# Kernel tuning notes

Hardware: AMD Instinct MI355X
Metric: run time of the kernel (lower is better)

## Reference

```python
import jax, jax.numpy as jnp
import numpy as np

B, S, H = 4, 1024, 1024
NH, HD = 16, 64  # num heads, head dim


def setup_inputs() -> dict:
    key = jax.random.key(0)
    ks = jax.random.split(key, 7)
    scale = 1.0 / np.sqrt(H)
    return {
        "hidden_states": jax.random.normal(ks[0], (B, S, H), jnp.float32),
        "attention_mask": jnp.zeros((B, 1, 1, S), jnp.float32),
        "Wq": jax.random.normal(ks[1], (H, H), jnp.float32) * scale,
        "bq": jnp.zeros((H,), jnp.float32),
        "Wk": jax.random.normal(ks[2], (H, H), jnp.float32) * scale,
        "bk": jnp.zeros((H,), jnp.float32),
        "Wv": jax.random.normal(ks[3], (H, H), jnp.float32) * scale,
        "bv": jnp.zeros((H,), jnp.float32),
    }


def _heads(x):
    # [B,S,H] -> [B,NH,S,HD]
    return x.reshape(x.shape[0], x.shape[1], NH, HD).transpose(0, 2, 1, 3)


def reference(hidden_states, attention_mask, Wq, bq, Wk, bk, Wv, bv):
    q = _heads(hidden_states @ Wq + bq)  # [B,NH,S,HD]
    k = _heads(hidden_states @ Wk + bk)
    v = _heads(hidden_states @ Wv + bv)
    scores = jnp.einsum("bhqd,bhkd->bhqk", q, k) / np.sqrt(HD)
    scores = scores + attention_mask  # broadcast additive mask
    probs = jax.nn.softmax(scores, axis=-1)  # dropout p=0 (eval)
    ctx = jnp.einsum("bhqk,bhkd->bhqd", probs, v)
    # [B,NH,S,HD] -> [B,S,H]
    return ctx.transpose(0, 2, 1, 3).reshape(hidden_states.shape[0], hidden_states.shape[1], NH * HD)
```

## Files before the change

kernel.cpp:

```cpp
#include <hip/hip_runtime.h>
#include <hip/hip_bf16.h>

typedef __bf16 bf16_t;
typedef __bf16 bf16x8 __attribute__((ext_vector_type(8)));
typedef float f32x4 __attribute__((ext_vector_type(4)));
typedef float f32x8 __attribute__((ext_vector_type(8)));
typedef float f32x16 __attribute__((ext_vector_type(16)));
typedef unsigned uint2v __attribute__((ext_vector_type(2)));

#define MFMA16(a, b, c) __builtin_amdgcn_mfma_f32_16x16x32_bf16((a), (b), (c), 0, 0, 0)
#define MFMA32(a, b, c) __builtin_amdgcn_mfma_f32_32x32x16_bf16((a), (b), (c), 0, 0, 0)

static constexpr int BB = 4, SS = 1024, HH = 1024, NHEAD = 16, HDIM = 64;
static constexpr int MM = BB * SS;

__device__ __forceinline__ void gload_lds16(const void* g, void* l) {
  __builtin_amdgcn_global_load_lds((const __attribute__((address_space(1))) void*)g,
                                   (__attribute__((address_space(3))) void*)l, 16, 0, 0);
}

#if __has_builtin(__builtin_amdgcn_permlane32_swap)
#define PSWAP(a, b)                                                    \
  {                                                                    \
    uint2v _r = __builtin_amdgcn_permlane32_swap((a), (b), false, false); \
    (a) = _r.x;                                                        \
    (b) = _r.y;                                                        \
  }
#else
#define PSWAP(a, b) asm("v_permlane32_swap_b32 %0, %1" : "+v"(a), "+v"(b))
#endif

__device__ __forceinline__ float EXP2(float x) {
  float r;
  asm("v_exp_f32 %0, %1" : "=v"(r) : "v"(x));
  return r;
}

__global__ __launch_bounds__(256) void prep_kernel(const float* __restrict__ hs,
                                                   const float* __restrict__ Wq,
                                                   const float* __restrict__ Wk,
                                                   const float* __restrict__ Wv,
                                                   bf16_t* __restrict__ hiddenB,
                                                   bf16_t* __restrict__ WT) {
  const int t = threadIdx.x;
  if (blockIdx.x < 2048) {
    int i = (blockIdx.x * 256 + t) * 8;
    float4 a = *(const float4*)(hs + i);
    float4 b = *(const float4*)(hs + i + 4);
    union { int4 i4; bf16_t h[8]; } u;
    u.h[0] = (bf16_t)a.x; u.h[1] = (bf16_t)a.y; u.h[2] = (bf16_t)a.z; u.h[3] = (bf16_t)a.w;
    u.h[4] = (bf16_t)b.x; u.h[5] = (bf16_t)b.y; u.h[6] = (bf16_t)b.z; u.h[7] = (bf16_t)b.w;
    *(int4*)(hiddenB + i) = u.i4;
  } else {
    __shared__ float tile[32][33];
    int id = blockIdx.x - 2048;
    int z = id >> 10;
    int rem = id & 1023;
    int bx = rem & 31, by = rem >> 5;
    const float* W = (z == 0) ? Wq : (z == 1) ? Wk : Wv;
    bf16_t* Out = WT + (size_t)z * HH * HH;
    int tx = t & 31, ty = t >> 5;
    int x0 = bx * 32;
    int y0 = by * 32;
    for (int j = ty; j < 32; j += 8)
      tile[j][tx] = W[(size_t)(y0 + j) * HH + x0 + tx];
    __syncthreads();
    for (int j = ty; j < 32; j += 8)
      Out[(size_t)(x0 + j) * HH + y0 + tx] = (bf16_t)tile[tx][j];
  }
}

#define BMT 128
#define BNT 384
#define BKT 64
#define NTL 16
#define BUFBYTES 65536

__global__ __launch_bounds__(512, 2) void qkv_gemm5(const bf16_t* __restrict__ hiddenB,
                                                    const bf16_t* __restrict__ WT,
                                                    const float* __restrict__ bq,
                                                    const float* __restrict__ bk,
                                                    const float* __restrict__ bv,
                                                    bf16_t* __restrict__ Qo,
                                                    bf16_t* __restrict__ Ko,
                                                    bf16_t* __restrict__ Vt) {
  __shared__ bf16_t smem[2 * BUFBYTES / 2];

  const int wg = blockIdx.x;
  const int id = (wg & 7) * 32 + (wg >> 3);
  const int nb = id & 7;
  const int mb = id >> 3;

  const int t = threadIdx.x;
  const int lane = t & 63;
  const int w = t >> 6;
  const int wr = w >> 2;
  const int wc = w & 3;
  const int lr = lane & 15;
  const int g4 = lane >> 4;

  const unsigned schunk = (((unsigned)(t & 7)) ^ ((unsigned)((t >> 3) & 7))) << 4;
  const char* Ag = (const char*)hiddenB + (size_t)(mb * BMT) * 2048;
  const char* Bg = (const char*)WT + (size_t)(nb * BNT) * 2048;

  auto stage = [&](const char* gb, int growbase, int kbyte, char* ldsdest) {
    gload_lds16(gb + (size_t)(growbase + (t >> 3)) * 2048 + kbyte + schunk,
                ldsdest + w * 1024);
  };
  const unsigned axor = ((unsigned)(lr & 7)) << 4;

  auto rdA = [&](const char* Ab, int mi, int ks) -> bf16x8 {
    return *(const bf16x8*)(Ab + (size_t)(wr * 64 + mi * 16 + lr) * 128 +
                            (((unsigned)(ks * 64 + g4 * 16)) ^ axor));
  };
  auto rdB = [&](const char* Bb, int p, int ni, int ks) -> bf16x8 {
    return *(const bf16x8*)(Bb + (size_t)(p * 128 + wc * 32 + ni * 16 + lr) * 128 +
                            (((unsigned)(ks * 64 + g4 * 16)) ^ axor));
  };

  f32x4 acc[4][6] = {};

  {
    char* S0 = (char*)smem;
    stage(Ag, 0, 0, S0); stage(Ag, 64, 0, S0 + 8192);
#pragma unroll
    for (int i = 0; i < 6; ++i) stage(Bg, i * 64, 0, S0 + 16384 + i * 8192);
    char* S1 = (char*)smem + BUFBYTES;
    stage(Ag, 0, 128, S1); stage(Ag, 64, 128, S1 + 8192);
#pragma unroll
    for (int i = 0; i < 6; ++i) stage(Bg, i * 64, 128, S1 + 16384 + i * 8192);
  }
  asm volatile("s_waitcnt vmcnt(8)" ::: "memory");
  __builtin_amdgcn_s_barrier();

  for (int j = 0; j < NTL; ++j) {
    const char* Ab = (const char*)smem + (j & 1) * BUFBYTES;
    const char* Bb = Ab + 16384;
    char* Sb = (char*)smem + (j & 1) * BUFBYTES;
    const bool st = (j + 2 < NTL);
    const int kb2 = (j + 2) * 128;

    bf16x8 af[4][2], b0[2][2];
#pragma unroll
    for (int mi = 0; mi < 4; ++mi)
#pragma unroll
      for (int ks = 0; ks < 2; ++ks) af[mi][ks] = rdA(Ab, mi, ks);
#pragma unroll
    for (int ni = 0; ni < 2; ++ni)
#pragma unroll
      for (int ks = 0; ks < 2; ++ks) b0[ni][ks] = rdB(Bb, 0, ni, ks);
    asm volatile("s_waitcnt lgkmcnt(0)" ::: "memory");
    __builtin_amdgcn_s_barrier();
    if (st) {
      stage(Ag, 0, kb2, Sb); stage(Ag, 64, kb2, Sb + 8192);
      stage(Bg, 0, kb2, Sb + 16384); stage(Bg, 64, kb2, Sb + 16384 + 8192);
    }
    __builtin_amdgcn_s_setprio(1);
#pragma unroll
    for (int mi = 0; mi < 4; ++mi)
#pragma unroll
      for (int ni = 0; ni < 2; ++ni)
#pragma unroll
        for (int ks = 0; ks < 2; ++ks)
          acc[mi][ni] = MFMA16(af[mi][ks], b0[ni][ks], acc[mi][ni]);
    __builtin_amdgcn_s_setprio(0);

    bf16x8 b1[2][2];
#pragma unroll
    for (int ni = 0; ni < 2; ++ni)
#pragma unroll
      for (int ks = 0; ks < 2; ++ks) b1[ni][ks] = rdB(Bb, 1, ni, ks);
    asm volatile("s_waitcnt lgkmcnt(0)" ::: "memory");
    __builtin_amdgcn_s_barrier();
    if (st) {
      stage(Bg, 128, kb2, Sb + 16384 + 2 * 8192);
      stage(Bg, 192, kb2, Sb + 16384 + 3 * 8192);
    }
    __builtin_amdgcn_s_setprio(1);
#pragma unroll
    for (int mi = 0; mi < 4; ++mi)
#pragma unroll
      for (int ni = 0; ni < 2; ++ni)
#pragma unroll
        for (int ks = 0; ks < 2; ++ks)
          acc[mi][2 + ni] = MFMA16(af[mi][ks], b1[ni][ks], acc[mi][2 + ni]);
    __builtin_amdgcn_s_setprio(0);

    bf16x8 b2[2][2];
#pragma unroll
    for (int ni = 0; ni < 2; ++ni)
#pragma unroll
      for (int ks = 0; ks < 2; ++ks) b2[ni][ks] = rdB(Bb, 2, ni, ks);
    asm volatile("s_waitcnt lgkmcnt(0)" ::: "memory");
    __builtin_amdgcn_s_barrier();
    if (st) {
      stage(Bg, 256, kb2, Sb + 16384 + 4 * 8192);
      stage(Bg, 320, kb2, Sb + 16384 + 5 * 8192);
    }
    __builtin_amdgcn_s_setprio(1);
#pragma unroll
    for (int mi = 0; mi < 4; ++mi)
#pragma unroll
      for (int ni = 0; ni < 2; ++ni)
#pragma unroll
        for (int ks = 0; ks < 2; ++ks)
          acc[mi][4 + ni] = MFMA16(af[mi][ks], b2[ni][ks], acc[mi][4 + ni]);
    __builtin_amdgcn_s_setprio(0);

    if (j + 1 < NTL) {
      if (st)
        asm volatile("s_waitcnt vmcnt(8)" ::: "memory");
      else
        asm volatile("s_waitcnt vmcnt(0)" ::: "memory");
      __builtin_amdgcn_s_barrier();
    }
  }

#pragma unroll
  for (int ni6 = 0; ni6 < 6; ++ni6) {
    int p = ni6 >> 1, ni = ni6 & 1;
    int col = nb * BNT + p * 128 + wc * 32 + ni * 16 + lr;
    int z = col >> 10;
    int ci = col & 1023;
    const float* bias = (z == 0) ? bq : (z == 1) ? bk : bv;
    float bia = bias[ci];
    int hh = ci >> 6, d = ci & 63;
    if (z < 2) {
      bf16_t* Out = (z == 0) ? Qo : Ko;
#pragma unroll
      for (int mi = 0; mi < 4; ++mi) {
#pragma unroll
        for (int r = 0; r < 4; ++r) {
          int row = mb * BMT + wr * 64 + mi * 16 + g4 * 4 + r;
          int b = row >> 10, s = row & 1023;
          Out[((size_t)(b * NHEAD + hh) * SS + s) * HDIM + d] = (bf16_t)(acc[mi][ni6][r] + bia);
        }
      }
    } else {
#pragma unroll
      for (int mi = 0; mi < 4; ++mi) {
        int row0 = mb * BMT + wr * 64 + mi * 16 + g4 * 4;
        int b = row0 >> 10, s0 = row0 & 1023;
        float v0 = acc[mi][ni6][0] + bia, v1 = acc[mi][ni6][1] + bia;
        float v2 = acc[mi][ni6][2] + bia, v3 = acc[mi][ni6][3] + bia;
        unsigned u0, u1;
        asm("v_cvt_pk_bf16_f32 %0, %1, %2" : "=v"(u0) : "v"(v0), "v"(v1));
        asm("v_cvt_pk_bf16_f32 %0, %1, %2" : "=v"(u1) : "v"(v2), "v"(v3));
        uint2 pv; pv.x = u0; pv.y = u1;
        *(uint2*)&Vt[((size_t)(b * NHEAD + hh) * HDIM + d) * SS + s0] = pv;
      }
    }
  }
}

__global__ __launch_bounds__(512, 4) void attn8_kernel(const bf16_t* __restrict__ Q,
                                                       const bf16_t* __restrict__ K,
                                                       const bf16_t* __restrict__ Vt,
                                                       const float* __restrict__ mask,
                                                       float* __restrict__ out) {
  __shared__ bf16_t KVsm[2][2][2][64 * 64];
  __shared__ float Msm[SS];

  const int wg = blockIdx.x;
  const int id = (wg & 7) * 64 + (wg >> 3);
  const int xblk = id & 7;
  const int bh = id >> 3;

  const int b = bh >> 4;
  const int h = bh & 15;
  const int t = threadIdx.x;
  const int lane = t & 63;
  const int w = t >> 6;
  const int wl = w & 3;
  const int half = w >> 2;
  const int l31 = lane & 31;
  const int hi = lane >> 5;
  const int q0 = xblk * 128 + wl * 32;
  const int kvbase = half * 512;

  const bf16_t* Qh = Q + (size_t)bh * SS * HDIM;
  const bf16_t* Kh = K + (size_t)bh * SS * HDIM;
  const bf16_t* Vh = Vt + (size_t)bh * HDIM * SS;

  const float L2E = 1.4426950408889634f;
  if (t < 256) {
    float4 mv = *(const float4*)&mask[(size_t)b * SS + t * 4];
    mv.x = mv.x * L2E - 16.f; mv.y = mv.y * L2E - 16.f;
    mv.z = mv.z * L2E - 16.f; mv.w = mv.w * L2E - 16.f;
    *(float4*)&Msm[t * 4] = mv;
  }

  bf16x8 qb[4];
#pragma unroll
  for (int c = 0; c < 4; ++c) {
    bf16x8 q = *(const bf16x8*)&Qh[(size_t)(q0 + l31) * HDIM + c * 16 + hi * 8];
#pragma unroll
    for (int e = 0; e < 8; ++e) q[e] = (bf16_t)((float)q[e] * (0.125f * L2E));
    qb[c] = q;
  }

  const int srow = lane >> 3;
  const unsigned gcol = ((lane & 7) * 16) ^ (srow << 4);
  const unsigned swz = (unsigned)((l31 & 7) << 4);

  auto stageKV = [&](int tile, int buf) {
    const int kv0 = kvbase + tile * 64;
#pragma unroll
    for (int i = 0; i < 2; ++i) {
      int rbase = wl * 16 + i * 8;
      gload_lds16((const char*)Kh + (size_t)(kv0 + rbase + srow) * 128 + gcol,
                  (char*)&KVsm[half][buf][0][0] + (size_t)rbase * 128);
      gload_lds16((const char*)Vh + (size_t)(rbase + srow) * 2048 + (size_t)kv0 * 2 + gcol,
                  (char*)&KVsm[half][buf][1][0] + (size_t)rbase * 128);
    }
  };

  f32x16 acc0 = {}, acc1 = {};
  f32x8 la = {}, lb = {};

  stageKV(0, 0);
  asm volatile("s_waitcnt vmcnt(0) lgkmcnt(0)" ::: "memory");
  __builtin_amdgcn_s_barrier();

  for (int tt = 0; tt < 8; ++tt) {
    if (tt + 1 < 8) stageKV(tt + 1, (tt + 1) & 1);
    const char* Kb = (const char*)&KVsm[half][tt & 1][0][0];
    const char* Vb = (const char*)&KVsm[half][tt & 1][1][0];
    const int kv0 = kvbase + tt * 64;

    f32x16 st0 = {}, st1 = {};
    __builtin_amdgcn_s_setprio(1);
#pragma unroll
    for (int c = 0; c < 4; ++c) {
      bf16x8 kf0 = *(const bf16x8*)(Kb + (size_t)l31 * 128 + ((unsigned)(c * 32 + hi * 16) ^ swz));
      st0 = MFMA32(kf0, qb[c], st0);
    }
#pragma unroll
    for (int c = 0; c < 4; ++c) {
      bf16x8 kf1 = *(const bf16x8*)(Kb + (size_t)(32 + l31) * 128 + ((unsigned)(c * 32 + hi * 16) ^ swz));
      st1 = MFMA32(kf1, qb[c], st1);
    }
    __builtin_amdgcn_s_setprio(0);

#pragma unroll
    for (int k2 = 0; k2 < 8; ++k2) {
      int off = 8 * (k2 >> 1) + 4 * hi + 2 * (k2 & 1);
      float2 m0v = *(const float2*)&Msm[kv0 + off];
      float2 m1v = *(const float2*)&Msm[kv0 + 32 + off];
      st0[2 * k2] += m0v.x; st0[2 * k2 + 1] += m0v.y;
      st1[2 * k2] += m1v.x; st1[2 * k2 + 1] += m1v.y;
    }
#pragma unroll
    for (int r = 0; r < 16; ++r) st0[r] = EXP2(st0[r]);
#pragma unroll
    for (int r = 0; r < 16; ++r) st1[r] = EXP2(st1[r]);

#pragma unroll
    for (int r = 0; r < 8; ++r) {
      la[r] += st0[r] + st0[r + 8];
      lb[r] += st1[r] + st1[r + 8];
    }

    unsigned wd0[8], wd1[8];
#pragma unroll
    for (int k2 = 0; k2 < 8; ++k2) {
      unsigned r0, r1;
      float a0f = st0[2 * k2], a1f = st0[2 * k2 + 1];
      float b0f = st1[2 * k2], b1f = st1[2 * k2 + 1];
      asm("v_cvt_pk_bf16_f32 %0, %1, %2" : "=v"(r0) : "v"(a0f), "v"(a1f));
      asm("v_cvt_pk_bf16_f32 %0, %1, %2" : "=v"(r1) : "v"(b0f), "v"(b1f));
      wd0[k2] = r0; wd1[k2] = r1;
    }
    unsigned a0 = wd0[0], b0 = wd0[2]; PSWAP(a0, b0);
    unsigned a1 = wd0[1], b1 = wd0[3]; PSWAP(a1, b1);
    unsigned a2 = wd0[4], b2 = wd0[6]; PSWAP(a2, b2);
    unsigned a3 = wd0[5], b3 = wd0[7]; PSWAP(a3, b3);
    unsigned c0 = wd1[0], d0 = wd1[2]; PSWAP(c0, d0);
    unsigned c1 = wd1[1], d1 = wd1[3]; PSWAP(c1, d1);
    unsigned c2 = wd1[4], d2 = wd1[6]; PSWAP(c2, d2);
    unsigned c3 = wd1[5], d3 = wd1[7]; PSWAP(c3, d3);
    union { unsigned u[4]; bf16x8 v; } pf0, pf1, pf2, pf3;
    pf0.u[0] = a0; pf0.u[1] = a1; pf0.u[2] = b0; pf0.u[3] = b1;
    pf1.u[0] = a2; pf1.u[1] = a3; pf1.u[2] = b2; pf1.u[3] = b3;
    pf2.u[0] = c0; pf2.u[1] = c1; pf2.u[2] = d0; pf2.u[3] = d1;
    pf3.u[0] = c2; pf3.u[1] = c3; pf3.u[2] = d2; pf3.u[3] = d3;

    __builtin_amdgcn_s_setprio(1);
    {
      bf16x8 vf;
      vf = *(const bf16x8*)(Vb + (size_t)(l31) * 128 + ((unsigned)(0 * 32 + hi * 16) ^ swz));
      acc0 = MFMA32(vf, pf0.v, acc0);
      vf = *(const bf16x8*)(Vb + (size_t)(32 + l31) * 128 + ((unsigned)(0 * 32 + hi * 16) ^ swz));
      acc1 = MFMA32(vf, pf0.v, acc1);
      vf = *(const bf16x8*)(Vb + (size_t)(l31) * 128 + ((unsigned)(1 * 32 + hi * 16) ^ swz));
      acc0 = MFMA32(vf, pf1.v, acc0);
      vf = *(const bf16x8*)(Vb + (size_t)(32 + l31) * 128 + ((unsigned)(1 * 32 + hi * 16) ^ swz));
      acc1 = MFMA32(vf, pf1.v, acc1);
      vf = *(const bf16x8*)(Vb + (size_t)(l31) * 128 + ((unsigned)(2 * 32 + hi * 16) ^ swz));
      acc0 = MFMA32(vf, pf2.v, acc0);
      vf = *(const bf16x8*)(Vb + (size_t)(32 + l31) * 128 + ((unsigned)(2 * 32 + hi * 16) ^ swz));
      acc1 = MFMA32(vf, pf2.v, acc1);
      vf = *(const bf16x8*)(Vb + (size_t)(l31) * 128 + ((unsigned)(3 * 32 + hi * 16) ^ swz));
      acc0 = MFMA32(vf, pf3.v, acc0);
      vf = *(const bf16x8*)(Vb + (size_t)(32 + l31) * 128 + ((unsigned)(3 * 32 + hi * 16) ^ swz));
      acc1 = MFMA32(vf, pf3.v, acc1);
    }
    __builtin_amdgcn_s_setprio(0);

    asm volatile("s_waitcnt vmcnt(0)" ::: "memory");
    __builtin_amdgcn_s_barrier();
  }

  float l_run;
  {
    float s0 = (la[0] + lb[0]) + (la[1] + lb[1]);
    float s1 = (la[2] + lb[2]) + (la[3] + lb[3]);
    float s2 = (la[4] + lb[4]) + (la[5] + lb[5]);
    float s3 = (la[6] + lb[6]) + (la[7] + lb[7]);
    l_run = (s0 + s1) + (s2 + s3);
    l_run += __shfl_xor(l_run, 32);
  }

  __syncthreads();
  float* mb = (float*)&KVsm[0][0][0][0];
  if (half == 1) {
    float* dst = mb + ((size_t)(wl * 64 + lane)) * 36;
#pragma unroll
    for (int g = 0; g < 4; ++g) {
      float4 w0, w1;
      w0.x = acc0[g * 4 + 0]; w0.y = acc0[g * 4 + 1];
      w0.z = acc0[g * 4 + 2]; w0.w = acc0[g * 4 + 3];
      w1.x = acc1[g * 4 + 0]; w1.y = acc1[g * 4 + 1];
      w1.z = acc1[g * 4 + 2]; w1.w = acc1[g * 4 + 3];
      *(float4*)(dst + g * 4) = w0;
      *(float4*)(dst + 16 + g * 4) = w1;
    }
    dst[32] = l_run;
  }
  __syncthreads();
  if (half == 0) {
    const float* src = mb + ((size_t)(wl * 64 + lane)) * 36;
    float rinv = 1.0f / (l_run + src[32]);
    int q = q0 + l31;
    float* ob = out + ((size_t)(b * SS + q)) * HH + h * HDIM;
#pragma unroll
    for (int g = 0; g < 4; ++g) {
      float4 o0, o1;
      o0.x = (acc0[g * 4 + 0] + src[g * 4 + 0]) * rinv;
      o0.y = (acc0[g * 4 + 1] + src[g * 4 + 1]) * rinv;
      o0.z = (acc0[g * 4 + 2] + src[g * 4 + 2]) * rinv;
      o0.w = (acc0[g * 4 + 3] + src[g * 4 + 3]) * rinv;
      o1.x = (acc1[g * 4 + 0] + src[16 + g * 4 + 0]) * rinv;
      o1.y = (acc1[g * 4 + 1] + src[16 + g * 4 + 1]) * rinv;
      o1.z = (acc1[g * 4 + 2] + src[16 + g * 4 + 2]) * rinv;
      o1.w = (acc1[g * 4 + 3] + src[16 + g * 4 + 3]) * rinv;
      *(float4*)&ob[g * 8 + 4 * hi] = o0;
      *(float4*)&ob[32 + g * 8 + 4 * hi] = o1;
    }
  }
}

extern "C" void kernel_launch(void* const* d_in, const int* in_sizes, int n_in,
                              void* d_out, int out_size, void* d_ws, size_t ws_size,
                              hipStream_t stream) {
  const float* hs   = (const float*)d_in[0];
  const float* mask = (const float*)d_in[1];
  const float* Wq   = (const float*)d_in[2];
  const float* bq   = (const float*)d_in[3];
  const float* Wk   = (const float*)d_in[4];
  const float* bk   = (const float*)d_in[5];
  const float* Wv   = (const float*)d_in[6];
  const float* bv   = (const float*)d_in[7];
  float* out = (float*)d_out;

  char* ws = (char*)d_ws;
  bf16_t* hiddenB = (bf16_t*)ws;
  bf16_t* WT      = (bf16_t*)(ws + (size_t)8 * 1024 * 1024);
  bf16_t* Qb      = (bf16_t*)(ws + (size_t)14 * 1024 * 1024);
  bf16_t* Kb      = (bf16_t*)(ws + (size_t)22 * 1024 * 1024);
  bf16_t* Vt      = (bf16_t*)(ws + (size_t)30 * 1024 * 1024);

  prep_kernel<<<2048 + 3072, 256, 0, stream>>>(hs, Wq, Wk, Wv, hiddenB, WT);
  qkv_gemm5<<<256, 512, 0, stream>>>(hiddenB, WT, bq, bk, bv, Qb, Kb, Vt);
  attn8_kernel<<<512, 512, 0, stream>>>(Qb, Kb, Vt, mask, out);
}
```

Measured before the change: 70.79 us.

## Fuse fp32-to-bf16 conversion of hidden states into the QKV GEMM loader

The hidden-state conversion pass is removed from the prep kernel. The QKV GEMM now loads fp32 activations directly into registers, converts them to bf16 with packed cvt instructions, and writes them into swizzled LDS, while B tiles keep using direct global-to-LDS loads. This avoids a separate write and re-read of an 8 MB bf16 intermediate. In exchange the GEMM reads twice as many A bytes, holds extra registers for the in-flight fp32 data, and adjusts its vmcnt wait counts.

```diff
diff --git a/kernel.cpp b/kernel.cpp
--- a/kernel.cpp
+++ b/kernel.cpp
@@ -35,48 +35,40 @@
   asm("v_exp_f32 %0, %1" : "=v"(r) : "v"(x));
   return r;
 }
-
-__global__ __launch_bounds__(256) void prep_kernel(const float* __restrict__ hs,
-                                                   const float* __restrict__ Wq,
-                                                   const float* __restrict__ Wk,
-                                                   const float* __restrict__ Wv,
-                                                   bf16_t* __restrict__ hiddenB,
-                                                   bf16_t* __restrict__ WT) {
+__device__ __forceinline__ unsigned CVTPK(float lo, float hi) {
+  unsigned r;
+  asm("v_cvt_pk_bf16_f32 %0, %1, %2" : "=v"(r) : "v"(lo), "v"(hi));
+  return r;
+}
+
+__global__ __launch_bounds__(256) void prepW_kernel(const float* __restrict__ Wq,
+                                                    const float* __restrict__ Wk,
+                                                    const float* __restrict__ Wv,
+                                                    bf16_t* __restrict__ WT) {
+  __shared__ float tile[32][33];
   const int t = threadIdx.x;
-  if (blockIdx.x < 2048) {
-    int i = (blockIdx.x * 256 + t) * 8;
-    float4 a = *(const float4*)(hs + i);
-    float4 b = *(const float4*)(hs + i + 4);
-    union { int4 i4; bf16_t h[8]; } u;
-    u.h[0] = (bf16_t)a.x; u.h[1] = (bf16_t)a.y; u.h[2] = (bf16_t)a.z; u.h[3] = (bf16_t)a.w;
-    u.h[4] = (bf16_t)b.x; u.h[5] = (bf16_t)b.y; u.h[6] = (bf16_t)b.z; u.h[7] = (bf16_t)b.w;
-    *(int4*)(hiddenB + i) = u.i4;
-  } else {
-    __shared__ float tile[32][33];
-    int id = blockIdx.x - 2048;
-    int z = id >> 10;
-    int rem = id & 1023;
-    int bx = rem & 31, by = rem >> 5;
-    const float* W = (z == 0) ? Wq : (z == 1) ? Wk : Wv;
-    bf16_t* Out = WT + (size_t)z * HH * HH;
-    int tx = t & 31, ty = t >> 5;
-    int x0 = bx * 32;
-    int y0 = by * 32;
-    for (int j = ty; j < 32; j += 8)
-      tile[j][tx] = W[(size_t)(y0 + j) * HH + x0 + tx];
-    __syncthreads();
-    for (int j = ty; j < 32; j += 8)
-      Out[(size_t)(x0 + j) * HH + y0 + tx] = (bf16_t)tile[tx][j];
-  }
+  int id = blockIdx.x;
+  int z = id >> 10;
+  int rem = id & 1023;
+  int bx = rem & 31, by = rem >> 5;
+  const float* W = (z == 0) ? Wq : (z == 1) ? Wk : Wv;
+  bf16_t* Out = WT + (size_t)z * HH * HH;
+  int tx = t & 31, ty = t >> 5;
+  int x0 = bx * 32;
+  int y0 = by * 32;
+  for (int j = ty; j < 32; j += 8)
+    tile[j][tx] = W[(size_t)(y0 + j) * HH + x0 + tx];
+  __syncthreads();
+  for (int j = ty; j < 32; j += 8)
+    Out[(size_t)(x0 + j) * HH + y0 + tx] = (bf16_t)tile[tx][j];
 }
 
 #define BMT 128
 #define BNT 384
-#define BKT 64
 #define NTL 16
 #define BUFBYTES 65536
 
-__global__ __launch_bounds__(512, 2) void qkv_gemm5(const bf16_t* __restrict__ hiddenB,
+__global__ __launch_bounds__(512, 2) void qkv_gemm6(const float* __restrict__ hs,
                                                     const bf16_t* __restrict__ WT,
                                                     const float* __restrict__ bq,
                                                     const float* __restrict__ bk,
@@ -99,16 +91,31 @@
   const int lr = lane & 15;
   const int g4 = lane >> 4;
 
-  const unsigned schunk = (((unsigned)(t & 7)) ^ ((unsigned)((t >> 3) & 7))) << 4;
-  const char* Ag = (const char*)hiddenB + (size_t)(mb * BMT) * 2048;
+  const int srow8 = t >> 3;
+  const int chunk = t & 7;
+  const unsigned schunk = (((unsigned)chunk) ^ ((unsigned)(srow8 & 7))) << 4;
+  const char* Ag32 = (const char*)hs + (size_t)(mb * BMT) * 4096;
   const char* Bg = (const char*)WT + (size_t)(nb * BNT) * 2048;
 
-  auto stage = [&](const char* gb, int growbase, int kbyte, char* ldsdest) {
-    gload_lds16(gb + (size_t)(growbase + (t >> 3)) * 2048 + kbyte + schunk,
+  auto stageB = [&](int growbase, int kbyte, char* ldsdest) {
+    gload_lds16(Bg + (size_t)(growbase + srow8) * 2048 + kbyte + schunk,
                 ldsdest + w * 1024);
   };
+  auto loadA = [&](int u, int kt, float4* dst) {
+    const char* p = Ag32 + (size_t)(u * 64 + srow8) * 4096 + (size_t)kt * 256 + chunk * 32;
+    dst[0] = *(const float4*)p;
+    dst[1] = *(const float4*)(p + 16);
+  };
+  auto writeA = [&](int u, const float4* a, char* SbA) {
+    uint4 wv;
+    wv.x = CVTPK(a[0].x, a[0].y);
+    wv.y = CVTPK(a[0].z, a[0].w);
+    wv.z = CVTPK(a[1].x, a[1].y);
+    wv.w = CVTPK(a[1].z, a[1].w);
+    *(uint4*)(SbA + (size_t)u * 8192 + (size_t)srow8 * 128 + schunk) = wv;
+  };
+
   const unsigned axor = ((unsigned)(lr & 7)) << 4;
-
   auto rdA = [&](const char* Ab, int mi, int ks) -> bf16x8 {
     return *(const bf16x8*)(Ab + (size_t)(wr * 64 + mi * 16 + lr) * 128 +
                             (((unsigned)(ks * 64 + g4 * 16)) ^ axor));
@@ -121,17 +128,21 @@
   f32x4 acc[4][6] = {};
 
   {
+    float4 pa0[2][2], pa1[2][2];
+    loadA(0, 0, pa0[0]); loadA(1, 0, pa0[1]);
+    loadA(0, 1, pa1[0]); loadA(1, 1, pa1[1]);
     char* S0 = (char*)smem;
-    stage(Ag, 0, 0, S0); stage(Ag, 64, 0, S0 + 8192);
-#pragma unroll
-    for (int i = 0; i < 6; ++i) stage(Bg, i * 64, 0, S0 + 16384 + i * 8192);
     char* S1 = (char*)smem + BUFBYTES;
-    stage(Ag, 0, 128, S1); stage(Ag, 64, 128, S1 + 8192);
-#pragma unroll
-    for (int i = 0; i < 6; ++i) stage(Bg, i * 64, 128, S1 + 16384 + i * 8192);
-  }
-  asm volatile("s_waitcnt vmcnt(8)" ::: "memory");
-  __builtin_amdgcn_s_barrier();
+#pragma unroll
+    for (int i = 0; i < 6; ++i) stageB(i * 64, 0, S0 + 16384 + i * 8192);
+#pragma unroll
+    for (int i = 0; i < 6; ++i) stageB(i * 64, 128, S1 + 16384 + i * 8192);
+    writeA(0, pa0[0], S0); writeA(1, pa0[1], S0);
+    writeA(0, pa1[0], S1); writeA(1, pa1[1], S1);
+    asm volatile("s_waitcnt lgkmcnt(0)" ::: "memory");
+    asm volatile("s_waitcnt vmcnt(6)" ::: "memory");
+    __builtin_amdgcn_s_barrier();
+  }
 
   for (int j = 0; j < NTL; ++j) {
     const char* Ab = (const char*)smem + (j & 1) * BUFBYTES;
@@ -140,6 +151,7 @@
     const bool st = (j + 2 < NTL);
     const int kb2 = (j + 2) * 128;
 
+    float4 a32[2][2];
     bf16x8 af[4][2], b0[2][2];
 #pragma unroll
     for (int mi = 0; mi < 4; ++mi)
@@ -152,8 +164,9 @@
     asm volatile("s_waitcnt lgkmcnt(0)" ::: "memory");
     __builtin_amdgcn_s_barrier();
     if (st) {
-      stage(Ag, 0, kb2, Sb); stage(Ag, 64, kb2, Sb + 8192);
-      stage(Bg, 0, kb2, Sb + 16384); stage(Bg, 64, kb2, Sb + 16384 + 8192);
+      loadA(0, j + 2, a32[0]);
+      loadA(1, j + 2, a32[1]);
+      stageB(0, kb2, Sb + 16384); stageB(64, kb2, Sb + 16384 + 8192);
     }
     __builtin_amdgcn_s_setprio(1);
 #pragma unroll
@@ -173,8 +186,8 @@
     asm volatile("s_waitcnt lgkmcnt(0)" ::: "memory");
     __builtin_amdgcn_s_barrier();
     if (st) {
-      stage(Bg, 128, kb2, Sb + 16384 + 2 * 8192);
-      stage(Bg, 192, kb2, Sb + 16384 + 3 * 8192);
+      stageB(128, kb2, Sb + 16384 + 2 * 8192);
+      stageB(192, kb2, Sb + 16384 + 3 * 8192);
     }
     __builtin_amdgcn_s_setprio(1);
 #pragma unroll
@@ -194,8 +207,10 @@
     asm volatile("s_waitcnt lgkmcnt(0)" ::: "memory");
     __builtin_amdgcn_s_barrier();
     if (st) {
-      stage(Bg, 256, kb2, Sb + 16384 + 4 * 8192);
-      stage(Bg, 320, kb2, Sb + 16384 + 5 * 8192);
+      stageB(256, kb2, Sb + 16384 + 4 * 8192);
+      stageB(320, kb2, Sb + 16384 + 5 * 8192);
+      writeA(0, a32[0], Sb);
+      writeA(1, a32[1], Sb);
     }
     __builtin_amdgcn_s_setprio(1);
 #pragma unroll
@@ -209,7 +224,7 @@
 
     if (j + 1 < NTL) {
       if (st)
-        asm volatile("s_waitcnt vmcnt(8)" ::: "memory");
+        asm volatile("s_waitcnt vmcnt(6)" ::: "memory");
       else
         asm volatile("s_waitcnt vmcnt(0)" ::: "memory");
       __builtin_amdgcn_s_barrier();
@@ -243,10 +258,9 @@
         int b = row0 >> 10, s0 = row0 & 1023;
         float v0 = acc[mi][ni6][0] + bia, v1 = acc[mi][ni6][1] + bia;
         float v2 = acc[mi][ni6][2] + bia, v3 = acc[mi][ni6][3] + bia;
-        unsigned u0, u1;
-        asm("v_cvt_pk_bf16_f32 %0, %1, %2" : "=v"(u0) : "v"(v0), "v"(v1));
-        asm("v_cvt_pk_bf16_f32 %0, %1, %2" : "=v"(u1) : "v"(v2), "v"(v3));
-        uint2 pv; pv.x = u0; pv.y = u1;
+        uint2 pv;
+        pv.x = CVTPK(v0, v1);
+        pv.y = CVTPK(v2, v3);
         *(uint2*)&Vt[((size_t)(b * NHEAD + hh) * HDIM + d) * SS + s0] = pv;
       }
     }
@@ -364,12 +378,8 @@
     unsigned wd0[8], wd1[8];
 #pragma unroll
     for (int k2 = 0; k2 < 8; ++k2) {
-      unsigned r0, r1;
-      float a0f = st0[2 * k2], a1f = st0[2 * k2 + 1];
-      float b0f = st1[2 * k2], b1f = st1[2 * k2 + 1];
-      asm("v_cvt_pk_bf16_f32 %0, %1, %2" : "=v"(r0) : "v"(a0f), "v"(a1f));
-      asm("v_cvt_pk_bf16_f32 %0, %1, %2" : "=v"(r1) : "v"(b0f), "v"(b1f));
-      wd0[k2] = r0; wd1[k2] = r1;
+      wd0[k2] = CVTPK(st0[2 * k2], st0[2 * k2 + 1]);
+      wd1[k2] = CVTPK(st1[2 * k2], st1[2 * k2 + 1]);
     }
     unsigned a0 = wd0[0], b0 = wd0[2]; PSWAP(a0, b0);
     unsigned a1 = wd0[1], b1 = wd0[3]; PSWAP(a1, b1);
@@ -422,9 +432,9 @@
   }
 
   __syncthreads();
-  float* mb = (float*)&KVsm[0][0][0][0];
+  float* mb2 = (float*)&KVsm[0][0][0][0];
   if (half == 1) {
-    float* dst = mb + ((size_t)(wl * 64 + lane)) * 36;
+    float* dst = mb2 + ((size_t)(wl * 64 + lane)) * 36;
 #pragma unroll
     for (int g = 0; g < 4; ++g) {
       float4 w0, w1;
@@ -439,7 +449,7 @@
   }
   __syncthreads();
   if (half == 0) {
-    const float* src = mb + ((size_t)(wl * 64 + lane)) * 36;
+    const float* src = mb2 + ((size_t)(wl * 64 + lane)) * 36;
     float rinv = 1.0f / (l_run + src[32]);
     int q = q0 + l31;
     float* ob = out + ((size_t)(b * SS + q)) * HH + h * HDIM;
@@ -474,13 +484,12 @@
   float* out = (float*)d_out;
 
   char* ws = (char*)d_ws;
-  bf16_t* hiddenB = (bf16_t*)ws;
   bf16_t* WT      = (bf16_t*)(ws + (size_t)8 * 1024 * 1024);
   bf16_t* Qb      = (bf16_t*)(ws + (size_t)14 * 1024 * 1024);
   bf16_t* Kb      = (bf16_t*)(ws + (size_t)22 * 1024 * 1024);
   bf16_t* Vt      = (bf16_t*)(ws + (size_t)30 * 1024 * 1024);
 
-  prep_kernel<<<2048 + 3072, 256, 0, stream>>>(hs, Wq, Wk, Wv, hiddenB, WT);
-  qkv_gemm5<<<256, 512, 0, stream>>>(hiddenB, WT, bq, bk, bv, Qb, Kb, Vt);
+  prepW_kernel<<<3072, 256, 0, stream>>>(Wq, Wk, Wv, WT);
+  qkv_gemm6<<<256, 512, 0, stream>>>(hs, WT, bq, bk, bv, Qb, Kb, Vt);
   attn8_kernel<<<512, 512, 0, stream>>>(Qb, Kb, Vt, mask, out);
 }
```

After: 80.44 us. 1.14x slower.
